# Optimization experiments

Hardware: AMD Instinct MI355X
Metric: run time of the kernel (lower is better)

The kernel has to match this reference:

```python
import jax, jax.numpy as jnp
import numpy as np

EPS = 1e-5


def _selective_scan(u, delta, A, Bm, Cm, D, delta_bias):
    # u, delta: (B, KD, L); A: (KD, N); Bm, Cm: (B, K, N, L); D, delta_bias: (KD,)
    Bb, KD, L = u.shape
    K = Bm.shape[1]
    Din = KD // K
    N = A.shape[1]
    delta = jax.nn.softplus(delta + delta_bias[None, :, None])            # (B,KD,L)
    dA = jnp.exp(delta[..., None] * A[None, :, None, :])                  # (B,KD,L,N)
    Bl = jnp.broadcast_to(Bm[:, :, None], (Bb, K, Din, N, L)).reshape(Bb, KD, N, L)
    Bl = jnp.moveaxis(Bl, -1, 2)                                          # (B,KD,L,N)
    dBu = (delta * u)[..., None] * Bl                                     # (B,KD,L,N)

    def comb(c1, c2):
        a1, b1 = c1
        a2, b2 = c2
        return a2 * a1, a2 * b1 + b2

    _, h = jax.lax.associative_scan(comb, (dA, dBu), axis=2)              # h: (B,KD,L,N)
    Cl = jnp.broadcast_to(Cm[:, :, None], (Bb, K, Din, N, L)).reshape(Bb, KD, N, L)
    Cl = jnp.moveaxis(Cl, -1, 2)
    y = jnp.sum(h * Cl, axis=-1) + D[None, :, None] * u                   # (B,KD,L)
    return y


def setup_inputs() -> dict:
    key = jax.random.key(0)
    ks = jax.random.split(key, 12)
    B, H, W, Dd = 1, 16, 16, 16
    C = 48            # d_model
    Din = 48          # d_inner (expand=1)
    N = 16            # d_state
    R = 3             # dt_rank = ceil(48/16)
    K = 8             # scan directions
    x = jax.random.normal(ks[0], (B, H, W, Dd, C), jnp.float32)
    in_proj_w = jax.random.normal(ks[1], (2 * Din, C), jnp.float32) * (C ** -0.5)
    conv_w = jax.random.normal(ks[2], (Din, 1, 3, 3, 3), jnp.float32) * 0.1
    conv_b = jax.random.normal(ks[3], (Din,), jnp.float32) * 0.01
    x_proj_weight = jax.random.normal(ks[4], (K, R + 2 * N, Din), jnp.float32) * (Din ** -0.5)
    dt_projs_weight = jax.random.uniform(ks[5], (K, Din, R), jnp.float32, -(R ** -0.5), R ** -0.5)
    # faithful dt bias init: inverse softplus of dt ~ logU(1e-3, 1e-1)
    u = jax.random.uniform(ks[6], (K, Din), jnp.float32)
    dt = jnp.exp(u * (np.log(0.1) - np.log(0.001)) + np.log(0.001))
    dt = jnp.clip(dt, 1e-4, None)
    dt_projs_bias = dt + jnp.log(-jnp.expm1(-dt))
    A_logs = jnp.log(jnp.broadcast_to(jnp.arange(1, N + 1, dtype=jnp.float32), (K * Din, N))).copy()
    Ds = jnp.ones((K * Din,), jnp.float32)
    norm_w = jnp.ones((Din,), jnp.float32)
    norm_b = jnp.zeros((Din,), jnp.float32)
    out_proj_w = jax.random.normal(ks[7], (C, Din), jnp.float32) * (Din ** -0.5)
    return {"x": x, "in_proj_w": in_proj_w, "conv_w": conv_w, "conv_b": conv_b,
            "x_proj_weight": x_proj_weight, "dt_projs_weight": dt_projs_weight,
            "dt_projs_bias": dt_projs_bias, "A_logs": A_logs, "Ds": Ds,
            "norm_w": norm_w, "norm_b": norm_b, "out_proj_w": out_proj_w}


def reference(x, in_proj_w, conv_w, conv_b, x_proj_weight, dt_projs_weight,
              dt_projs_bias, A_logs, Ds, norm_w, norm_b, out_proj_w):
    Bb, H, W, Dd, C = x.shape
    Din = in_proj_w.shape[0] // 2
    K = x_proj_weight.shape[0]
    R = dt_projs_weight.shape[2]
    N = A_logs.shape[1]
    L = H * W * Dd
    # in_proj and gate split
    xz = jnp.einsum('bhwdc,ec->bhwde', x, in_proj_w)
    xm, z = jnp.split(xz, 2, axis=-1)
    # depthwise 3D conv + SiLU (channels-first)
    xc = jnp.transpose(xm, (0, 4, 1, 2, 3))                               # (B,Din,H,W,D)
    xc = jax.lax.conv_general_dilated(xc, conv_w, (1, 1, 1), 'SAME',
                                      dimension_numbers=('NCDHW', 'OIDHW', 'NCDHW'),
                                      feature_group_count=Din)
    xc = jax.nn.silu(xc + conv_b[None, :, None, None, None])
    # 8 scan orderings: 4 axis permutations + their reversals
    x0 = xc.reshape(Bb, Din, L)
    x1 = jnp.transpose(xc, (0, 1, 3, 2, 4)).reshape(Bb, Din, L)
    x2 = jnp.transpose(xc, (0, 1, 4, 3, 2)).reshape(Bb, Din, L)
    x3 = jnp.transpose(xc, (0, 1, 2, 4, 3)).reshape(Bb, Din, L)
    x4s = jnp.stack([x0, x1, x2, x3], axis=1)                             # (B,4,Din,L)
    xs = jnp.concatenate([x4s, jnp.flip(x4s, axis=-1)], axis=1)           # (B,8,Din,L)
    # per-direction projections
    x_dbl = jnp.einsum('bkdl,kcd->bkcl', xs, x_proj_weight)
    dts, Bs, Cs = jnp.split(x_dbl, [R, R + N], axis=2)                    # (B,K,R,L),(B,K,N,L),(B,K,N,L)
    dts = jnp.einsum('bkrl,kdr->bkdl', dts, dt_projs_weight)              # (B,K,Din,L)
    u = xs.reshape(Bb, K * Din, L)
    delta = dts.reshape(Bb, K * Din, L)
    A = -jnp.exp(A_logs)                                                  # (K*Din, N)
    y = _selective_scan(u, delta, A, Bs, Cs, Ds, dt_projs_bias.reshape(-1))
    y = y.reshape(Bb, K, Din, L)
    # undo reversals and permutations, sum all directions
    yk = y[:, :4] + jnp.flip(y[:, 4:], axis=-1)                           # (B,4,Din,L)
    y0 = yk[:, 0].reshape(Bb, Din, H, W, Dd)
    y1 = jnp.transpose(yk[:, 1].reshape(Bb, Din, W, H, Dd), (0, 1, 3, 2, 4))
    y2 = jnp.transpose(yk[:, 2].reshape(Bb, Din, Dd, W, H), (0, 1, 4, 3, 2))
    y3 = jnp.transpose(yk[:, 3].reshape(Bb, Din, H, Dd, W), (0, 1, 2, 4, 3))
    ysum = y0 + y1 + y2 + y3                                              # (B,Din,H,W,D)
    # LayerNorm over channels, gate, out_proj
    yl = jnp.transpose(ysum, (0, 2, 3, 4, 1))                             # (B,H,W,D,Din)
    mu = jnp.mean(yl, axis=-1, keepdims=True)
    var = jnp.mean((yl - mu) ** 2, axis=-1, keepdims=True)
    yn = (yl - mu) * jax.lax.rsqrt(var + EPS) * norm_w + norm_b
    out = yn * jax.nn.silu(z)
    return jnp.einsum('bhwde,ce->bhwdc', out, out_proj_w)
```

## Files before the change

kernel.cpp:

```cpp
#include <hip/hip_runtime.h>
#include <math.h>

#define HH 16
#define WW 16
#define DD 16
#define LL 4096
#define CC 48
#define DIN 48
#define NN 16
#define RR 3
#define KK 8
#define KD 384
#define NCH 64
#define CHL 64

#define OL(s) ((s) + ((s) >> 4) + ((s) >> 8))

__device__ __forceinline__ float dpp_add(float x, const int ctrl_tag) {
    int xi = __float_as_int(x);
    int yi;
    switch (ctrl_tag) {
        case 0: yi = __builtin_amdgcn_update_dpp(0, xi, 0xB1, 0xF, 0xF, true); break;
        case 1: yi = __builtin_amdgcn_update_dpp(0, xi, 0x4E, 0xF, 0xF, true); break;
        case 2: yi = __builtin_amdgcn_update_dpp(0, xi, 0x124, 0xF, 0xF, true); break;
        default: yi = __builtin_amdgcn_update_dpp(0, xi, 0x128, 0xF, 0xF, true); break;
    }
    return x + __int_as_float(yi);
}
__device__ __forceinline__ float row16_sum(float p) {
    p = dpp_add(p, 0);
    p = dpp_add(p, 1);
    p = dpp_add(p, 2);
    p = dpp_add(p, 3);
    return p;
}

__device__ __forceinline__ int perm_src(int ll, int kperm) {
    int a = ll >> 8, b2 = (ll >> 4) & 15, c2 = ll & 15;
    switch (kperm) {
        case 0:  return ll;
        case 1:  return b2 * 256 + a * 16 + c2;
        case 2:  return c2 * 256 + b2 * 16 + a;
        default: return a * 256 + c2 * 16 + b2;
    }
}

__global__ __launch_bounds__(256) void k_inproj(const float* __restrict__ x,
                                                const float* __restrict__ W,
                                                float* __restrict__ xm,
                                                float* __restrict__ z) {
    int tid = blockIdx.x * 256 + threadIdx.x;
    if (tid >= LL * 96) return;
    int e = tid % 96, l = tid / 96;
    const float4* xr = (const float4*)(x + l * CC);
    const float4* wr = (const float4*)(W + e * CC);
    float acc = 0.f;
#pragma unroll
    for (int c4 = 0; c4 < CC / 4; ++c4) {
        float4 a = xr[c4], b = wr[c4];
        acc += a.x * b.x + a.y * b.y + a.z * b.z + a.w * b.w;
    }
    if (e < DIN) xm[e * LL + l] = acc;
    else         z[l * DIN + (e - DIN)] = acc;
}

__global__ __launch_bounds__(1024) void k_conv(const float* __restrict__ xm,
                                               const float* __restrict__ cw,
                                               const float* __restrict__ cb,
                                               float* __restrict__ xcp) {
    int d = blockIdx.x;
    int tid = threadIdx.x;
    __shared__ float xin[4366];
    __shared__ float xout[4366];
    {
        float4 v = ((const float4*)(xm + (size_t)d * LL))[tid];
        int o = OL(tid * 4);
        xin[o] = v.x; xin[o + 1] = v.y; xin[o + 2] = v.z; xin[o + 3] = v.w;
    }
    __syncthreads();
    const float* wp = cw + d * 27;
    float bias = cb[d];
#pragma unroll
    for (int j = 0; j < 4; ++j) {
        int s = tid * 4 + j;
        int dd = s & 15, w = (s >> 4) & 15, h = s >> 8;
        float acc = 0.f;
#pragma unroll
        for (int i = -1; i <= 1; ++i) {
            int hh = h + i; if (hh < 0 || hh > 15) continue;
#pragma unroll
            for (int jj = -1; jj <= 1; ++jj) {
                int ww2 = w + jj; if (ww2 < 0 || ww2 > 15) continue;
#pragma unroll
                for (int q = -1; q <= 1; ++q) {
                    int dd2 = dd + q; if (dd2 < 0 || dd2 > 15) continue;
                    acc += wp[(i + 1) * 9 + (jj + 1) * 3 + (q + 1)]
                         * xin[OL(hh * 256 + ww2 * 16 + dd2)];
                }
            }
        }
        acc += bias;
        xout[OL(s)] = acc / (1.f + __expf(-acc));
    }
    __syncthreads();
#pragma unroll
    for (int p = 0; p < 4; ++p) {
        float4 v;
#pragma unroll
        for (int j = 0; j < 4; ++j) {
            int lp = tid * 4 + j;
            (&v.x)[j] = xout[OL(perm_src(lp, p))];
        }
        ((float4*)(xcp + ((size_t)p * DIN + d) * LL))[tid] = v;
    }
}

__device__ __forceinline__ void frontend(const float* __restrict__ xcp,
                                         const float* __restrict__ xpw,
                                         const float* __restrict__ dtw,
                                         const float* __restrict__ dtb,
                                         int k, int l0, int tid,
                                         float* xt, float* xd, float2* ud) {
    int kperm = k & 3, krev = k & 4;
    {
        int d = tid >> 4, q = tid & 15;
        const float* row = xcp + ((size_t)kperm * DIN + d) * LL;
        if (!krev) {
            float4 v = ((const float4*)(row + l0))[q];
            xt[d * 68 + q * 4 + 0] = v.x; xt[d * 68 + q * 4 + 1] = v.y;
            xt[d * 68 + q * 4 + 2] = v.z; xt[d * 68 + q * 4 + 3] = v.w;
        } else {
            float4 v = ((const float4*)(row + (LL - CHL - l0)))[15 - q];
            xt[d * 68 + q * 4 + 3] = v.x; xt[d * 68 + q * 4 + 2] = v.y;
            xt[d * 68 + q * 4 + 1] = v.z; xt[d * 68 + q * 4 + 0] = v.w;
        }
    }
    __syncthreads();
    if (tid < 560) {
        int cc = tid % 35, l4 = tid / 35;
        const float* wr = xpw + (k * 35 + cc) * DIN;
        float4 acc = {0.f, 0.f, 0.f, 0.f};
#pragma unroll
        for (int d2 = 0; d2 < 48; ++d2) {
            float4 v = ((const float4*)(xt + d2 * 68))[l4];
            float w = wr[d2];
            acc.x += v.x * w; acc.y += v.y * w; acc.z += v.z * w; acc.w += v.w * w;
        }
        float* o = xd + cc * 65 + l4 * 4;
        o[0] = acc.x; o[1] = acc.y; o[2] = acc.z; o[3] = acc.w;
    }
    __syncthreads();
#pragma unroll
    for (int r = 0; r < 4; ++r) {
        int item = r * 768 + tid;
        int d2 = item >> 6, l = item & 63;
        int gd = k * DIN + d2;
        float v = xd[l] * dtw[gd * 3] + xd[65 + l] * dtw[gd * 3 + 1]
                + xd[130 + l] * dtw[gd * 3 + 2] + dtb[gd];
        float sp = (v > 20.f) ? v : log1pf(__expf(v));
        ud[d2 * 68 + l] = make_float2(xt[d2 * 68 + l], sp);
    }
    __syncthreads();
}

__global__ __launch_bounds__(768) void k_scanA(const float* __restrict__ xcp,
                                               const float* __restrict__ xpw,
                                               const float* __restrict__ dtw,
                                               const float* __restrict__ dtb,
                                               const float* __restrict__ A_logs,
                                               float* __restrict__ phf_g) {
    int k = blockIdx.x >> 6;
    int c = blockIdx.x & (NCH - 1);
    int l0 = c * CHL;
    int tid = threadIdx.x;
    __shared__ float  xt[48 * 68];
    __shared__ float  xd[35 * 65];
    __shared__ float2 ud[48 * 68];
    frontend(xcp, xpw, dtw, dtb, k, l0, tid, xt, xd, ud);
    int d = tid >> 4, n = tid & 15;
    int gid = k * DIN + d;
    float A = -__expf(A_logs[gid * NN + n]);
    float h = 0.f, pa = 1.f;
#pragma unroll 8
    for (int i = 0; i < CHL; ++i) {
        float2 uv = ud[d * 68 + i];
        float Bv = xd[(3 + n) * 65 + i];
        float dA = __expf(uv.y * A);
        h = h * dA + uv.y * uv.x * Bv;
        pa *= dA;
    }
    ((float2*)phf_g)[(size_t)gid * (NCH * 16) + c * 16 + n] = make_float2(pa, h);
}

__global__ __launch_bounds__(768) void k_scanB(const float* __restrict__ xcp,
                                               const float* __restrict__ xpw,
                                               const float* __restrict__ dtw,
                                               const float* __restrict__ dtb,
                                               const float* __restrict__ A_logs,
                                               const float* __restrict__ Ds,
                                               const float* __restrict__ phf_g,
                                               float* __restrict__ y2) {
    int k = blockIdx.x >> 6;
    int c = blockIdx.x & (NCH - 1);
    int l0 = c * CHL;
    int tid = threadIdx.x;
    __shared__ float  xt[48 * 68];
    __shared__ float  xd[35 * 65];
    __shared__ float2 ud[48 * 68];
    frontend(xcp, xpw, dtw, dtb, k, l0, tid, xt, xd, ud);
    int d = tid >> 4, n = tid & 15;
    int gid = k * DIN + d;
    float A = -__expf(A_logs[gid * NN + n]);
    float Dv = Ds[gid];
    float h = 0.f;
    {
        const float2* pp = ((const float2*)phf_g) + (size_t)gid * (NCH * 16) + n;
        int cc = 0;
        for (; cc + 8 <= c; cc += 8) {
            float2 v0 = pp[(cc + 0) * 16]; float2 v1 = pp[(cc + 1) * 16];
            float2 v2 = pp[(cc + 2) * 16]; float2 v3 = pp[(cc + 3) * 16];
            float2 v4 = pp[(cc + 4) * 16]; float2 v5 = pp[(cc + 5) * 16];
            float2 v6 = pp[(cc + 6) * 16]; float2 v7 = pp[(cc + 7) * 16];
            h = h * v0.x + v0.y; h = h * v1.x + v1.y;
            h = h * v2.x + v2.y; h = h * v3.x + v3.y;
            h = h * v4.x + v4.y; h = h * v5.x + v5.y;
            h = h * v6.x + v6.y; h = h * v7.x + v7.y;
        }
        for (; cc < c; ++cc) { float2 v = pp[cc * 16]; h = h * v.x + v.y; }
    }
#pragma unroll 8
    for (int i = 0; i < CHL; ++i) {
        float2 uv = ud[d * 68 + i];
        float Bv = xd[(3 + n) * 65 + i];
        float Cv = xd[(19 + n) * 65 + i];
        float dA = __expf(uv.y * A);
        h = h * dA + uv.y * uv.x * Bv;
        float p = row16_sum(h * Cv);
        if (n == 0) xt[d * 68 + i] = p + Dv * uv.x;
    }
    __syncthreads();
    {
        int g = tid >> 6, l = tid & 63;
        int lg = l0 + l;
        int ll = (k & 4) ? (LL - 1 - lg) : lg;
        int sp = perm_src(ll, k & 3);
        float4 v;
#pragma unroll
        for (int j = 0; j < 4; ++j) (&v.x)[j] = xt[(g * 4 + j) * 68 + l];
        ((float4*)(y2 + (size_t)sp * KD + k * DIN))[g] = v;
    }
}

__global__ __launch_bounds__(256) void k_final2(const float* __restrict__ y2,
                                                const float* __restrict__ z,
                                                const float* __restrict__ nw,
                                                const float* __restrict__ nb,
                                                const float* __restrict__ opw,
                                                float* __restrict__ out) {
    int wv = threadIdx.x >> 6, lane = threadIdx.x & 63;
    int s = blockIdx.x * 4 + wv;
    __shared__ float g[4][DIN];
    float val = 0.f;
    if (lane < DIN) {
        const float* yp = y2 + (size_t)s * KD + lane;
#pragma unroll
        for (int k = 0; k < KK; ++k) val += yp[k * DIN];
    }
    float m = val;
#pragma unroll
    for (int o = 32; o >= 1; o >>= 1) m += __shfl_xor(m, o, 64);
    m *= (1.f / 48.f);
    float dv = (lane < DIN) ? (val - m) : 0.f;
    float v2 = dv * dv;
#pragma unroll
    for (int o = 32; o >= 1; o >>= 1) v2 += __shfl_xor(v2, o, 64);
    v2 *= (1.f / 48.f);
    float inv = rsqrtf(v2 + 1e-5f);
    if (lane < DIN) {
        float yn = dv * inv * nw[lane] + nb[lane];
        float zz = z[s * DIN + lane];
        g[wv][lane] = yn * (zz / (1.f + __expf(-zz)));
    }
    __syncthreads();
    if (lane < DIN) {
        const float* wr = opw + lane * DIN;
        float acc = 0.f;
#pragma unroll
        for (int e = 0; e < DIN; ++e) acc += g[wv][e] * wr[e];
        out[s * CC + lane] = acc;
    }
}

extern "C" void kernel_launch(void* const* d_in, const int* in_sizes, int n_in,
                              void* d_out, int out_size, void* d_ws, size_t ws_size,
                              hipStream_t stream) {
    const float* x      = (const float*)d_in[0];
    const float* ipw    = (const float*)d_in[1];
    const float* cw     = (const float*)d_in[2];
    const float* cb     = (const float*)d_in[3];
    const float* xpw    = (const float*)d_in[4];
    const float* dtw    = (const float*)d_in[5];
    const float* dtb    = (const float*)d_in[6];
    const float* A_logs = (const float*)d_in[7];
    const float* Ds     = (const float*)d_in[8];
    const float* nw     = (const float*)d_in[9];
    const float* nb     = (const float*)d_in[10];
    const float* opw    = (const float*)d_in[11];
    float* out = (float*)d_out;

    float* ws    = (float*)d_ws;
    float* xm    = ws;
    float* z     = xm + DIN * LL;
    float* xcp   = z + LL * DIN;
    float* y2    = xcp + (size_t)4 * DIN * LL;
    float* phf_g = y2 + (size_t)LL * KD;

    k_inproj<<<(LL * 96 + 255) / 256, 256, 0, stream>>>(x, ipw, xm, z);
    k_conv<<<DIN, 1024, 0, stream>>>(xm, cw, cb, xcp);
    k_scanA<<<KK * NCH, 768, 0, stream>>>(xcp, xpw, dtw, dtb, A_logs, phf_g);
    k_scanB<<<KK * NCH, 768, 0, stream>>>(xcp, xpw, dtw, dtb, A_logs, Ds,
                                          phf_g, y2);
    k_final2<<<LL / 4, 256, 0, stream>>>(y2, z, nw, nb, opw, out);
}
```

Before: 146.2 us.

## Fuse chunked scan passes into one kernel with decoupled chunk-prefix handoff

```diff
diff --git a/kernel.cpp b/kernel.cpp
--- a/kernel.cpp
+++ b/kernel.cpp
@@ -48,8 +48,16 @@
 __global__ __launch_bounds__(256) void k_inproj(const float* __restrict__ x,
                                                 const float* __restrict__ W,
                                                 float* __restrict__ xm,
-                                                float* __restrict__ z) {
+                                                float* __restrict__ z,
+                                                int* __restrict__ sync) {
     int tid = blockIdx.x * 256 + threadIdx.x;
+    if (blockIdx.x == 0 && threadIdx.x < 64) {
+#pragma unroll
+        for (int r = 0; r < 9; ++r) {
+            int i = r * 64 + threadIdx.x;
+            if (i < 513) sync[i] = 0;
+        }
+    }
     if (tid >= LL * 96) return;
     int e = tid % 96, l = tid / 96;
     const float4* xr = (const float4*)(x + l * CC);
@@ -163,70 +171,74 @@
     __syncthreads();
 }
 
-__global__ __launch_bounds__(768) void k_scanA(const float* __restrict__ xcp,
-                                               const float* __restrict__ xpw,
-                                               const float* __restrict__ dtw,
-                                               const float* __restrict__ dtb,
-                                               const float* __restrict__ A_logs,
-                                               float* __restrict__ phf_g) {
-    int k = blockIdx.x >> 6;
-    int c = blockIdx.x & (NCH - 1);
-    int l0 = c * CHL;
-    int tid = threadIdx.x;
+__global__ __launch_bounds__(768) void k_scanAB(
+        const float* __restrict__ xcp, const float* __restrict__ xpw,
+        const float* __restrict__ dtw, const float* __restrict__ dtb,
+        const float* __restrict__ A_logs, const float* __restrict__ Ds,
+        float2* __restrict__ phf, int* __restrict__ sync,
+        float* __restrict__ y2) {
     __shared__ float  xt[48 * 68];
     __shared__ float  xd[35 * 65];
     __shared__ float2 ud[48 * 68];
+    __shared__ int s_bid;
+    int tid = threadIdx.x;
+    if (tid == 0) s_bid = atomicAdd(&sync[0], 1);
+    __syncthreads();
+    int bid = s_bid;
+    int k = bid >> 6, c = bid & (NCH - 1);
+    int l0 = c * CHL;
     frontend(xcp, xpw, dtw, dtb, k, l0, tid, xt, xd, ud);
     int d = tid >> 4, n = tid & 15;
     int gid = k * DIN + d;
     float A = -__expf(A_logs[gid * NN + n]);
-    float h = 0.f, pa = 1.f;
+    float Dv = Ds[gid];
+    float h1 = 0.f, pa = 1.f;
 #pragma unroll 8
     for (int i = 0; i < CHL; ++i) {
         float2 uv = ud[d * 68 + i];
         float Bv = xd[(3 + n) * 65 + i];
         float dA = __expf(uv.y * A);
-        h = h * dA + uv.y * uv.x * Bv;
+        h1 = h1 * dA + uv.y * uv.x * Bv;
         pa *= dA;
     }
-    ((float2*)phf_g)[(size_t)gid * (NCH * 16) + c * 16 + n] = make_float2(pa, h);
-}
-
-__global__ __launch_bounds__(768) void k_scanB(const float* __restrict__ xcp,
-                                               const float* __restrict__ xpw,
-                                               const float* __restrict__ dtw,
-                                               const float* __restrict__ dtb,
-                                               const float* __restrict__ A_logs,
-                                               const float* __restrict__ Ds,
-                                               const float* __restrict__ phf_g,
-                                               float* __restrict__ y2) {
-    int k = blockIdx.x >> 6;
-    int c = blockIdx.x & (NCH - 1);
-    int l0 = c * CHL;
-    int tid = threadIdx.x;
-    __shared__ float  xt[48 * 68];
-    __shared__ float  xd[35 * 65];
-    __shared__ float2 ud[48 * 68];
-    frontend(xcp, xpw, dtw, dtb, k, l0, tid, xt, xd, ud);
-    int d = tid >> 4, n = tid & 15;
-    int gid = k * DIN + d;
-    float A = -__expf(A_logs[gid * NN + n]);
-    float Dv = Ds[gid];
+    phf[(size_t)bid * 768 + tid] = make_float2(pa, h1);
+    __syncthreads();
+    if (tid == 0) {
+        __threadfence();
+        __hip_atomic_store(&sync[1 + bid], 1, __ATOMIC_RELEASE,
+                           __HIP_MEMORY_SCOPE_AGENT);
+    }
+    if (tid < c) {
+        while (__hip_atomic_load(&sync[1 + (k << 6) + tid], __ATOMIC_RELAXED,
+                                 __HIP_MEMORY_SCOPE_AGENT) == 0) {
+            __builtin_amdgcn_s_sleep(2);
+        }
+    }
+    __syncthreads();
+    if (tid == 0) __threadfence();
+    __syncthreads();
     float h = 0.f;
     {
-        const float2* pp = ((const float2*)phf_g) + (size_t)gid * (NCH * 16) + n;
+        const float2* pp = phf + ((size_t)(k << 6)) * 768 + tid;
         int cc = 0;
         for (; cc + 8 <= c; cc += 8) {
-            float2 v0 = pp[(cc + 0) * 16]; float2 v1 = pp[(cc + 1) * 16];
-            float2 v2 = pp[(cc + 2) * 16]; float2 v3 = pp[(cc + 3) * 16];
-            float2 v4 = pp[(cc + 4) * 16]; float2 v5 = pp[(cc + 5) * 16];
-            float2 v6 = pp[(cc + 6) * 16]; float2 v7 = pp[(cc + 7) * 16];
+            float2 v0 = pp[(size_t)(cc + 0) * 768];
+            float2 v1 = pp[(size_t)(cc + 1) * 768];
+            float2 v2 = pp[(size_t)(cc + 2) * 768];
+            float2 v3 = pp[(size_t)(cc + 3) * 768];
+            float2 v4 = pp[(size_t)(cc + 4) * 768];
+            float2 v5 = pp[(size_t)(cc + 5) * 768];
+            float2 v6 = pp[(size_t)(cc + 6) * 768];
+            float2 v7 = pp[(size_t)(cc + 7) * 768];
             h = h * v0.x + v0.y; h = h * v1.x + v1.y;
             h = h * v2.x + v2.y; h = h * v3.x + v3.y;
             h = h * v4.x + v4.y; h = h * v5.x + v5.y;
             h = h * v6.x + v6.y; h = h * v7.x + v7.y;
         }
-        for (; cc < c; ++cc) { float2 v = pp[cc * 16]; h = h * v.x + v.y; }
+        for (; cc < c; ++cc) {
+            float2 v = pp[(size_t)cc * 768];
+            h = h * v.x + v.y;
+        }
     }
 #pragma unroll 8
     for (int i = 0; i < CHL; ++i) {
@@ -313,12 +325,12 @@
     float* z     = xm + DIN * LL;
     float* xcp   = z + LL * DIN;
     float* y2    = xcp + (size_t)4 * DIN * LL;
-    float* phf_g = y2 + (size_t)LL * KD;
-
-    k_inproj<<<(LL * 96 + 255) / 256, 256, 0, stream>>>(x, ipw, xm, z);
+    float* phf_f = y2 + (size_t)LL * KD;
+    int*   sync  = (int*)(phf_f + (size_t)2 * 512 * 768);
+
+    k_inproj<<<(LL * 96 + 255) / 256, 256, 0, stream>>>(x, ipw, xm, z, sync);
     k_conv<<<DIN, 1024, 0, stream>>>(xm, cw, cb, xcp);
-    k_scanA<<<KK * NCH, 768, 0, stream>>>(xcp, xpw, dtw, dtb, A_logs, phf_g);
-    k_scanB<<<KK * NCH, 768, 0, stream>>>(xcp, xpw, dtw, dtb, A_logs, Ds,
-                                          phf_g, y2);
+    k_scanAB<<<KK * NCH, 768, 0, stream>>>(xcp, xpw, dtw, dtb, A_logs, Ds,
+                                           (float2*)phf_f, sync, y2);
     k_final2<<<LL / 4, 256, 0, stream>>>(y2, z, nw, nb, opw, out);
 }
```

After: 177.2 us. 21.3% more time.

## Compute local chunk scan output in pass A, apply carry correction in pass B

Applied to the files above, without the earlier changes.

```diff
diff --git a/kernel.cpp b/kernel.cpp
--- a/kernel.cpp
+++ b/kernel.cpp
@@ -115,12 +115,23 @@
     }
 }
 
-__device__ __forceinline__ void frontend(const float* __restrict__ xcp,
-                                         const float* __restrict__ xpw,
-                                         const float* __restrict__ dtw,
-                                         const float* __restrict__ dtb,
-                                         int k, int l0, int tid,
-                                         float* xt, float* xd, float2* ud) {
+__global__ __launch_bounds__(768) void k_scanA(const float* __restrict__ xcp,
+                                               const float* __restrict__ xpw,
+                                               const float* __restrict__ dtw,
+                                               const float* __restrict__ dtb,
+                                               const float* __restrict__ A_logs,
+                                               const float* __restrict__ Ds,
+                                               float* __restrict__ yl_g,
+                                               float* __restrict__ C_g,
+                                               float* __restrict__ phf_g) {
+    int k = blockIdx.x >> 6;
+    int c = blockIdx.x & (NCH - 1);
+    int l0 = c * CHL;
+    int tid = threadIdx.x;
+    __shared__ float  xt[48 * 68];
+    __shared__ float  xd[35 * 65];
+    __shared__ float2 ud[48 * 68];
+    __shared__ float2 yl[48 * 64];
     int kperm = k & 3, krev = k & 4;
     {
         int d = tid >> 4, q = tid & 15;
@@ -161,58 +172,65 @@
         ud[d2 * 68 + l] = make_float2(xt[d2 * 68 + l], sp);
     }
     __syncthreads();
-}
-
-__global__ __launch_bounds__(768) void k_scanA(const float* __restrict__ xcp,
-                                               const float* __restrict__ xpw,
-                                               const float* __restrict__ dtw,
-                                               const float* __restrict__ dtb,
-                                               const float* __restrict__ A_logs,
-                                               float* __restrict__ phf_g) {
-    int k = blockIdx.x >> 6;
-    int c = blockIdx.x & (NCH - 1);
-    int l0 = c * CHL;
-    int tid = threadIdx.x;
-    __shared__ float  xt[48 * 68];
-    __shared__ float  xd[35 * 65];
-    __shared__ float2 ud[48 * 68];
-    frontend(xcp, xpw, dtw, dtb, k, l0, tid, xt, xd, ud);
+    if (tid < 256) {
+        int l = tid >> 2, q = tid & 3;
+        float4 v;
+#pragma unroll
+        for (int j = 0; j < 4; ++j) (&v.x)[j] = xd[(19 + q * 4 + j) * 65 + l];
+        ((float4*)(C_g + ((size_t)(k * LL + l0 + l)) * 16))[q] = v;
+    }
     int d = tid >> 4, n = tid & 15;
     int gid = k * DIN + d;
     float A = -__expf(A_logs[gid * NN + n]);
-    float h = 0.f, pa = 1.f;
+    float Dv = Ds[gid];
+    float S = 0.f, cum = 0.f;
 #pragma unroll 8
     for (int i = 0; i < CHL; ++i) {
         float2 uv = ud[d * 68 + i];
         float Bv = xd[(3 + n) * 65 + i];
+        cum += uv.y;
         float dA = __expf(uv.y * A);
-        h = h * dA + uv.y * uv.x * Bv;
-        pa *= dA;
-    }
-    ((float2*)phf_g)[(size_t)gid * (NCH * 16) + c * 16 + n] = make_float2(pa, h);
-}
-
-__global__ __launch_bounds__(768) void k_scanB(const float* __restrict__ xcp,
-                                               const float* __restrict__ xpw,
-                                               const float* __restrict__ dtw,
-                                               const float* __restrict__ dtb,
+        S = S * dA + uv.y * uv.x * Bv;
+        float t = row16_sum(S * xd[(19 + n) * 65 + i]);
+        if (n == 0) yl[d * 64 + i] = make_float2(t + Dv * uv.x, cum);
+    }
+    ((float2*)phf_g)[(size_t)gid * (NCH * 16) + c * 16 + n] =
+        make_float2(__expf(A * cum), S);
+    __syncthreads();
+#pragma unroll
+    for (int r = 0; r < 2; ++r) {
+        int item = r * 768 + tid;
+        int d2 = item >> 5, q = item & 31;
+        ((float4*)yl_g)[((size_t)(k * DIN + d2) * LL + l0) / 2 + q] =
+            ((const float4*)yl)[d2 * 32 + q];
+    }
+}
+
+__global__ __launch_bounds__(768) void k_scanB(const float* __restrict__ yl_g,
+                                               const float* __restrict__ C_g,
                                                const float* __restrict__ A_logs,
-                                               const float* __restrict__ Ds,
                                                const float* __restrict__ phf_g,
                                                float* __restrict__ y2) {
     int k = blockIdx.x >> 6;
     int c = blockIdx.x & (NCH - 1);
     int l0 = c * CHL;
     int tid = threadIdx.x;
-    __shared__ float  xt[48 * 68];
-    __shared__ float  xd[35 * 65];
-    __shared__ float2 ud[48 * 68];
-    frontend(xcp, xpw, dtw, dtb, k, l0, tid, xt, xd, ud);
     int d = tid >> 4, n = tid & 15;
     int gid = k * DIN + d;
+    __shared__ float2 ylc[48 * 64];
+    __shared__ float  sc[64 * 16];
+    __shared__ float  y_t[48 * 68];
+#pragma unroll
+    for (int r = 0; r < 2; ++r) {
+        int item = r * 768 + tid;
+        int d2 = item >> 5, q = item & 31;
+        ((float4*)ylc)[d2 * 32 + q] =
+            ((const float4*)yl_g)[((size_t)(k * DIN + d2) * LL + l0) / 2 + q];
+    }
+    if (tid < 256)
+        ((float4*)sc)[tid] = ((const float4*)(C_g + (size_t)(k * LL + l0) * 16))[tid];
     float A = -__expf(A_logs[gid * NN + n]);
-    float Dv = Ds[gid];
-    float h = 0.f;
+    float h0 = 0.f;
     {
         const float2* pp = ((const float2*)phf_g) + (size_t)gid * (NCH * 16) + n;
         int cc = 0;
@@ -221,22 +239,20 @@
             float2 v2 = pp[(cc + 2) * 16]; float2 v3 = pp[(cc + 3) * 16];
             float2 v4 = pp[(cc + 4) * 16]; float2 v5 = pp[(cc + 5) * 16];
             float2 v6 = pp[(cc + 6) * 16]; float2 v7 = pp[(cc + 7) * 16];
-            h = h * v0.x + v0.y; h = h * v1.x + v1.y;
-            h = h * v2.x + v2.y; h = h * v3.x + v3.y;
-            h = h * v4.x + v4.y; h = h * v5.x + v5.y;
-            h = h * v6.x + v6.y; h = h * v7.x + v7.y;
-        }
-        for (; cc < c; ++cc) { float2 v = pp[cc * 16]; h = h * v.x + v.y; }
-    }
+            h0 = h0 * v0.x + v0.y; h0 = h0 * v1.x + v1.y;
+            h0 = h0 * v2.x + v2.y; h0 = h0 * v3.x + v3.y;
+            h0 = h0 * v4.x + v4.y; h0 = h0 * v5.x + v5.y;
+            h0 = h0 * v6.x + v6.y; h0 = h0 * v7.x + v7.y;
+        }
+        for (; cc < c; ++cc) { float2 v = pp[cc * 16]; h0 = h0 * v.x + v.y; }
+    }
+    __syncthreads();
 #pragma unroll 8
     for (int i = 0; i < CHL; ++i) {
-        float2 uv = ud[d * 68 + i];
-        float Bv = xd[(3 + n) * 65 + i];
-        float Cv = xd[(19 + n) * 65 + i];
-        float dA = __expf(uv.y * A);
-        h = h * dA + uv.y * uv.x * Bv;
-        float p = row16_sum(h * Cv);
-        if (n == 0) xt[d * 68 + i] = p + Dv * uv.x;
+        float2 yc = ylc[d * 64 + i];
+        float t = sc[i * 16 + n] * __expf(A * yc.y) * h0;
+        float s = row16_sum(t);
+        if (n == 0) y_t[d * 68 + i] = yc.x + s;
     }
     __syncthreads();
     {
@@ -246,7 +262,7 @@
         int sp = perm_src(ll, k & 3);
         float4 v;
 #pragma unroll
-        for (int j = 0; j < 4; ++j) (&v.x)[j] = xt[(g * 4 + j) * 68 + l];
+        for (int j = 0; j < 4; ++j) (&v.x)[j] = y_t[(g * 4 + j) * 68 + l];
         ((float4*)(y2 + (size_t)sp * KD + k * DIN))[g] = v;
     }
 }
@@ -313,12 +329,14 @@
     float* z     = xm + DIN * LL;
     float* xcp   = z + LL * DIN;
     float* y2    = xcp + (size_t)4 * DIN * LL;
-    float* phf_g = y2 + (size_t)LL * KD;
+    float* yl_g  = y2 + (size_t)LL * KD;
+    float* C_g   = yl_g + (size_t)2 * KD * LL;
+    float* phf_g = C_g + (size_t)KK * LL * 16;
 
     k_inproj<<<(LL * 96 + 255) / 256, 256, 0, stream>>>(x, ipw, xm, z);
     k_conv<<<DIN, 1024, 0, stream>>>(xm, cw, cb, xcp);
-    k_scanA<<<KK * NCH, 768, 0, stream>>>(xcp, xpw, dtw, dtb, A_logs, phf_g);
-    k_scanB<<<KK * NCH, 768, 0, stream>>>(xcp, xpw, dtw, dtb, A_logs, Ds,
-                                          phf_g, y2);
+    k_scanA<<<KK * NCH, 768, 0, stream>>>(xcp, xpw, dtw, dtb, A_logs, Ds,
+                                          yl_g, C_g, phf_g);
+    k_scanB<<<KK * NCH, 768, 0, stream>>>(yl_g, C_g, A_logs, phf_g, y2);
     k_final2<<<LL / 4, 256, 0, stream>>>(y2, z, nw, nb, opw, out);
 }
```

Result: slower. 149.1 us (+2.0%).

## Fuse in_proj into conv kernel and cache scan frontend outputs for second pass

Applied to the files above, without the earlier changes.

```diff
diff --git a/kernel.cpp b/kernel.cpp
--- a/kernel.cpp
+++ b/kernel.cpp
@@ -45,82 +45,114 @@
     }
 }
 
-__global__ __launch_bounds__(256) void k_inproj(const float* __restrict__ x,
-                                                const float* __restrict__ W,
-                                                float* __restrict__ xm,
+__global__ __launch_bounds__(1024) void k_front(const float* __restrict__ x,
+                                                const float* __restrict__ ipw,
+                                                const float* __restrict__ cw,
+                                                const float* __restrict__ cb,
+                                                float* __restrict__ xcp,
                                                 float* __restrict__ z) {
-    int tid = blockIdx.x * 256 + threadIdx.x;
-    if (tid >= LL * 96) return;
-    int e = tid % 96, l = tid / 96;
-    const float4* xr = (const float4*)(x + l * CC);
-    const float4* wr = (const float4*)(W + e * CC);
-    float acc = 0.f;
-#pragma unroll
-    for (int c4 = 0; c4 < CC / 4; ++c4) {
-        float4 a = xr[c4], b = wr[c4];
-        acc += a.x * b.x + a.y * b.y + a.z * b.z + a.w * b.w;
-    }
-    if (e < DIN) xm[e * LL + l] = acc;
-    else         z[l * DIN + (e - DIN)] = acc;
-}
-
-__global__ __launch_bounds__(1024) void k_conv(const float* __restrict__ xm,
-                                               const float* __restrict__ cw,
-                                               const float* __restrict__ cb,
-                                               float* __restrict__ xcp) {
-    int d = blockIdx.x;
     int tid = threadIdx.x;
-    __shared__ float xin[4366];
-    __shared__ float xout[4366];
-    {
-        float4 v = ((const float4*)(xm + (size_t)d * LL))[tid];
-        int o = OL(tid * 4);
-        xin[o] = v.x; xin[o + 1] = v.y; xin[o + 2] = v.z; xin[o + 3] = v.w;
-    }
-    __syncthreads();
-    const float* wp = cw + d * 27;
-    float bias = cb[d];
-#pragma unroll
-    for (int j = 0; j < 4; ++j) {
-        int s = tid * 4 + j;
-        int dd = s & 15, w = (s >> 4) & 15, h = s >> 8;
-        float acc = 0.f;
-#pragma unroll
-        for (int i = -1; i <= 1; ++i) {
-            int hh = h + i; if (hh < 0 || hh > 15) continue;
-#pragma unroll
-            for (int jj = -1; jj <= 1; ++jj) {
-                int ww2 = w + jj; if (ww2 < 0 || ww2 > 15) continue;
-#pragma unroll
-                for (int q = -1; q <= 1; ++q) {
-                    int dd2 = dd + q; if (dd2 < 0 || dd2 > 15) continue;
-                    acc += wp[(i + 1) * 9 + (jj + 1) * 3 + (q + 1)]
-                         * xin[OL(hh * 256 + ww2 * 16 + dd2)];
+    if (blockIdx.x < DIN) {
+        int d = blockIdx.x;
+        __shared__ float xin[4366];
+        __shared__ float xout[4366];
+        {
+            const float4* wr = (const float4*)(ipw + d * CC);
+            float4 w[12];
+#pragma unroll
+            for (int c4 = 0; c4 < 12; ++c4) w[c4] = wr[c4];
+#pragma unroll
+            for (int r = 0; r < 4; ++r) {
+                int l = r * 1024 + tid;
+                const float4* xr = (const float4*)(x + (size_t)l * CC);
+                float acc = 0.f;
+#pragma unroll
+                for (int c4 = 0; c4 < 12; ++c4) {
+                    float4 a = xr[c4];
+                    acc += a.x * w[c4].x + a.y * w[c4].y
+                         + a.z * w[c4].z + a.w * w[c4].w;
+                }
+                xin[OL(l)] = acc;
+            }
+        }
+        __syncthreads();
+        const float* wp = cw + d * 27;
+        float bias = cb[d];
+#pragma unroll
+        for (int j = 0; j < 4; ++j) {
+            int s = tid * 4 + j;
+            int dd = s & 15, w = (s >> 4) & 15, h = s >> 8;
+            float acc = 0.f;
+#pragma unroll
+            for (int i = -1; i <= 1; ++i) {
+                int hh = h + i; if (hh < 0 || hh > 15) continue;
+#pragma unroll
+                for (int jj = -1; jj <= 1; ++jj) {
+                    int ww2 = w + jj; if (ww2 < 0 || ww2 > 15) continue;
+#pragma unroll
+                    for (int q = -1; q <= 1; ++q) {
+                        int dd2 = dd + q; if (dd2 < 0 || dd2 > 15) continue;
+                        acc += wp[(i + 1) * 9 + (jj + 1) * 3 + (q + 1)]
+                             * xin[OL(hh * 256 + ww2 * 16 + dd2)];
+                    }
                 }
             }
-        }
-        acc += bias;
-        xout[OL(s)] = acc / (1.f + __expf(-acc));
-    }
-    __syncthreads();
-#pragma unroll
-    for (int p = 0; p < 4; ++p) {
-        float4 v;
-#pragma unroll
-        for (int j = 0; j < 4; ++j) {
-            int lp = tid * 4 + j;
-            (&v.x)[j] = xout[OL(perm_src(lp, p))];
-        }
-        ((float4*)(xcp + ((size_t)p * DIN + d) * LL))[tid] = v;
-    }
-}
-
-__device__ __forceinline__ void frontend(const float* __restrict__ xcp,
-                                         const float* __restrict__ xpw,
-                                         const float* __restrict__ dtw,
-                                         const float* __restrict__ dtb,
-                                         int k, int l0, int tid,
-                                         float* xt, float* xd, float2* ud) {
+            acc += bias;
+            xout[OL(s)] = acc / (1.f + __expf(-acc));
+        }
+        __syncthreads();
+#pragma unroll
+        for (int p = 0; p < 4; ++p) {
+            float4 v;
+#pragma unroll
+            for (int j = 0; j < 4; ++j) {
+                int lp = tid * 4 + j;
+                (&v.x)[j] = xout[OL(perm_src(lp, p))];
+            }
+            ((float4*)(xcp + ((size_t)p * DIN + d) * LL))[tid] = v;
+        }
+    } else {
+        int e0 = (blockIdx.x - DIN) * 4;
+#pragma unroll
+        for (int r = 0; r < 4; ++r) {
+            int l = r * 1024 + tid;
+            const float4* xr = (const float4*)(x + (size_t)l * CC);
+            float4 xv[12];
+#pragma unroll
+            for (int c4 = 0; c4 < 12; ++c4) xv[c4] = xr[c4];
+            float4 out;
+#pragma unroll
+            for (int j = 0; j < 4; ++j) {
+                const float4* wj = (const float4*)(ipw + (size_t)(DIN + e0 + j) * CC);
+                float acc = 0.f;
+#pragma unroll
+                for (int c4 = 0; c4 < 12; ++c4) {
+                    float4 b = wj[c4];
+                    acc += xv[c4].x * b.x + xv[c4].y * b.y
+                         + xv[c4].z * b.z + xv[c4].w * b.w;
+                }
+                (&out.x)[j] = acc;
+            }
+            *((float4*)(z + (size_t)l * DIN + e0)) = out;
+        }
+    }
+}
+
+__global__ __launch_bounds__(768) void k_scan1(const float* __restrict__ xcp,
+                                               const float* __restrict__ xpw,
+                                               const float* __restrict__ dtw,
+                                               const float* __restrict__ dtb,
+                                               const float* __restrict__ A_logs,
+                                               float* __restrict__ BC,
+                                               float* __restrict__ ud_g,
+                                               float* __restrict__ phf_g) {
+    int k = blockIdx.x >> 6;
+    int c = blockIdx.x & (NCH - 1);
+    int l0 = c * CHL;
+    int tid = threadIdx.x;
+    __shared__ float  xt[48 * 68];
+    __shared__ float  xd[35 * 65];
+    __shared__ float2 ud[48 * 68];
     int kperm = k & 3, krev = k & 4;
     {
         int d = tid >> 4, q = tid & 15;
@@ -150,6 +182,13 @@
         o[0] = acc.x; o[1] = acc.y; o[2] = acc.z; o[3] = acc.w;
     }
     __syncthreads();
+    if (tid < 512) {
+        int l = tid >> 3, q = tid & 7;
+        float4 v;
+#pragma unroll
+        for (int j = 0; j < 4; ++j) (&v.x)[j] = xd[(3 + q * 4 + j) * 65 + l];
+        ((float4*)(BC + ((size_t)(k * LL + l0 + l)) * 32))[q] = v;
+    }
 #pragma unroll
     for (int r = 0; r < 4; ++r) {
         int item = r * 768 + tid;
@@ -158,25 +197,12 @@
         float v = xd[l] * dtw[gd * 3] + xd[65 + l] * dtw[gd * 3 + 1]
                 + xd[130 + l] * dtw[gd * 3 + 2] + dtb[gd];
         float sp = (v > 20.f) ? v : log1pf(__expf(v));
-        ud[d2 * 68 + l] = make_float2(xt[d2 * 68 + l], sp);
-    }
-    __syncthreads();
-}
-
-__global__ __launch_bounds__(768) void k_scanA(const float* __restrict__ xcp,
-                                               const float* __restrict__ xpw,
-                                               const float* __restrict__ dtw,
-                                               const float* __restrict__ dtb,
-                                               const float* __restrict__ A_logs,
-                                               float* __restrict__ phf_g) {
-    int k = blockIdx.x >> 6;
-    int c = blockIdx.x & (NCH - 1);
-    int l0 = c * CHL;
-    int tid = threadIdx.x;
-    __shared__ float  xt[48 * 68];
-    __shared__ float  xd[35 * 65];
-    __shared__ float2 ud[48 * 68];
-    frontend(xcp, xpw, dtw, dtb, k, l0, tid, xt, xd, ud);
+        float u = xt[d2 * 68 + l];
+        float2 p = make_float2(u, sp);
+        ud[d2 * 68 + l] = p;
+        ((float2*)ud_g)[(size_t)gd * LL + l0 + l] = p;
+    }
+    __syncthreads();
     int d = tid >> 4, n = tid & 15;
     int gid = k * DIN + d;
     float A = -__expf(A_logs[gid * NN + n]);
@@ -192,26 +218,36 @@
     ((float2*)phf_g)[(size_t)gid * (NCH * 16) + c * 16 + n] = make_float2(pa, h);
 }
 
-__global__ __launch_bounds__(768) void k_scanB(const float* __restrict__ xcp,
-                                               const float* __restrict__ xpw,
-                                               const float* __restrict__ dtw,
-                                               const float* __restrict__ dtb,
-                                               const float* __restrict__ A_logs,
-                                               const float* __restrict__ Ds,
-                                               const float* __restrict__ phf_g,
-                                               float* __restrict__ y2) {
+__global__ __launch_bounds__(768, 6) void k_scan3(const float* __restrict__ ud_g,
+                                                  const float* __restrict__ BC,
+                                                  const float* __restrict__ A_logs,
+                                                  const float* __restrict__ Ds,
+                                                  const float* __restrict__ phf_g,
+                                                  float* __restrict__ y2) {
     int k = blockIdx.x >> 6;
     int c = blockIdx.x & (NCH - 1);
     int l0 = c * CHL;
     int tid = threadIdx.x;
-    __shared__ float  xt[48 * 68];
-    __shared__ float  xd[35 * 65];
-    __shared__ float2 ud[48 * 68];
-    frontend(xcp, xpw, dtw, dtb, k, l0, tid, xt, xd, ud);
     int d = tid >> 4, n = tid & 15;
     int gid = k * DIN + d;
+    __shared__ float2 s_ud[48 * 64];
+    __shared__ float  s_bc[64 * 32];
+    __shared__ float  y_t[48 * 68];
+
+    const float4* ud4 = (const float4*)ud_g;
+    const float4* bc4 = (const float4*)BC;
+    int r0 = tid >> 5, q0 = tid & 31;
+    float4 ua = ud4[(size_t)(k * DIN + r0)      * (LL / 2) + (l0 / 2) + q0];
+    float4 ub = ud4[(size_t)(k * DIN + 24 + r0) * (LL / 2) + (l0 / 2) + q0];
+    float4 bv;
+    if (tid < 512) bv = bc4[((size_t)(k * LL + l0 + (tid >> 3))) * 8 + (tid & 7)];
+    ((float4*)s_ud)[tid] = ua;
+    ((float4*)s_ud)[768 + tid] = ub;
+    if (tid < 512) ((float4*)s_bc)[tid] = bv;
+
     float A = -__expf(A_logs[gid * NN + n]);
     float Dv = Ds[gid];
+
     float h = 0.f;
     {
         const float2* pp = ((const float2*)phf_g) + (size_t)gid * (NCH * 16) + n;
@@ -228,15 +264,18 @@
         }
         for (; cc < c; ++cc) { float2 v = pp[cc * 16]; h = h * v.x + v.y; }
     }
+    __syncthreads();
+
+    const float2* ur = s_ud + d * 64;
 #pragma unroll 8
     for (int i = 0; i < CHL; ++i) {
-        float2 uv = ud[d * 68 + i];
-        float Bv = xd[(3 + n) * 65 + i];
-        float Cv = xd[(19 + n) * 65 + i];
+        float2 uv = ur[i];
+        float Bv = s_bc[i * 32 + n];
+        float Cv = s_bc[i * 32 + 16 + n];
         float dA = __expf(uv.y * A);
         h = h * dA + uv.y * uv.x * Bv;
         float p = row16_sum(h * Cv);
-        if (n == 0) xt[d * 68 + i] = p + Dv * uv.x;
+        if (n == 0) y_t[d * 68 + i] = p + Dv * uv.x;
     }
     __syncthreads();
     {
@@ -246,7 +285,7 @@
         int sp = perm_src(ll, k & 3);
         float4 v;
 #pragma unroll
-        for (int j = 0; j < 4; ++j) (&v.x)[j] = xt[(g * 4 + j) * 68 + l];
+        for (int j = 0; j < 4; ++j) (&v.x)[j] = y_t[(g * 4 + j) * 68 + l];
         ((float4*)(y2 + (size_t)sp * KD + k * DIN))[g] = v;
     }
 }
@@ -309,16 +348,16 @@
     float* out = (float*)d_out;
 
     float* ws    = (float*)d_ws;
-    float* xm    = ws;
-    float* z     = xm + DIN * LL;
-    float* xcp   = z + LL * DIN;
-    float* y2    = xcp + (size_t)4 * DIN * LL;
+    float* z     = ws;
+    float* xcp   = z + (size_t)LL * DIN;
+    float* ud_g  = xcp + (size_t)4 * DIN * LL;
+    float* BC    = ud_g + (size_t)2 * KD * LL;
+    float* y2    = BC + (size_t)KK * LL * 32;
     float* phf_g = y2 + (size_t)LL * KD;
 
-    k_inproj<<<(LL * 96 + 255) / 256, 256, 0, stream>>>(x, ipw, xm, z);
-    k_conv<<<DIN, 1024, 0, stream>>>(xm, cw, cb, xcp);
-    k_scanA<<<KK * NCH, 768, 0, stream>>>(xcp, xpw, dtw, dtb, A_logs, phf_g);
-    k_scanB<<<KK * NCH, 768, 0, stream>>>(xcp, xpw, dtw, dtb, A_logs, Ds,
-                                          phf_g, y2);
+    k_front<<<DIN + 12, 1024, 0, stream>>>(x, ipw, cw, cb, xcp, z);
+    k_scan1<<<KK * NCH, 768, 0, stream>>>(xcp, xpw, dtw, dtb, A_logs,
+                                          BC, ud_g, phf_g);
+    k_scan3<<<KK * NCH, 768, 0, stream>>>(ud_g, BC, A_logs, Ds, phf_g, y2);
     k_final2<<<LL / 4, 256, 0, stream>>>(y2, z, nw, nb, opw, out);
 }
```

Measured after the change: 147.2 us. About the same (+0.7%).
